# Kernel optimization log

Measured on AMD Instinct MI355X. Metric: run time of the kernel, lower is better.

## Reference

```python
import jax, jax.numpy as jnp
import numpy as np

ALPHA = 0.95   # membrane leak factor exp(-dt/tau_mem)
RHO   = 0.98   # threshold-adaptation decay
BETA  = 1.8    # adaptive threshold gain (ALIF)
TH0   = 1.0    # base threshold
SCALE = 10.0   # SuperSpike surrogate slope

@jax.custom_vjp
def spike(v):
    # Heaviside spike with SuperSpike surrogate gradient (as in cantata's SurrGradSpike)
    return (v >= 0.0).astype(v.dtype)

def _spike_fwd(v):
    return spike(v), v

def _spike_bwd(v, g):
    return (g / (SCALE * jnp.abs(v) + 1.0) ** 2,)

spike.defvjp(_spike_fwd, _spike_bwd)

def _onehot_delays(k, n, d):
    # each presynaptic source is routed through exactly one delay bin
    idx = jax.random.randint(k, (n,), 0, d)
    return (jnp.arange(d)[:, None] == idx[None, :]).astype(jnp.float32)  # [d, n]

def setup_inputs() -> dict:
    B, N, D, NE, DE = 32, 4096, 8, 2048, 4
    key = jax.random.key(0)
    ks = jax.random.split(key, 8)
    V = jax.random.normal(ks[0], (B, N), jnp.float32)
    a = jax.random.uniform(ks[1], (B, N), jnp.float32)
    Xd = (jax.random.uniform(ks[2], (D, B, N)) < 0.05).astype(jnp.float32)      # internal delay ring buffer
    Xext = (jax.random.uniform(ks[3], (DE, B, NE)) < 0.05).astype(jnp.float32)  # delayed external spikes
    W_int = jax.random.normal(ks[4], (N, N), jnp.float32) * 0.02
    W_ext = jax.random.normal(ks[5], (NE, N), jnp.float32) * 0.02
    dmap_int = _onehot_delays(ks[6], N, D)
    dmap_ext = _onehot_delays(ks[7], NE, DE)
    return dict(V=V, a=a, Xd=Xd, Xext=Xext, W_int=W_int, W_ext=W_ext,
                dmap_int=dmap_int, dmap_ext=dmap_ext)

def reference(V, a, Xd, Xext, W_int, W_ext, dmap_int, dmap_ext):
    # 1) ALIF spike generation from membrane + adaptive threshold
    th = TH0 + BETA * a
    X = spike(V - th)                                     # [B,N]
    a_new = RHO * a + X
    # 2) push new spikes into the delay ring buffer (delay 0 = current step)
    Xd_new = jnp.concatenate([X[None], Xd[:-1]], axis=0)  # [D,B,N]
    # 3) delay-mapped synaptic current: gather each presyn source from its delay bin,
    #    then dense delta-synapse accumulation (internal + cross-area)
    x_int = jnp.einsum('dbi,di->bi', Xd_new, dmap_int)    # [B,N]
    x_ext = jnp.einsum('dbi,di->bi', Xext, dmap_ext)      # [B,NE]
    current = x_int @ W_int + x_ext @ W_ext               # [B,N]
    # 4) membrane update: leak, reset on spike, integrate current
    V_new = ALPHA * V * (1.0 - X) + current
    return jnp.stack([X, V_new, a_new])                   # [3,B,N]
```

## Files before the change

kernel.cpp:

```cpp
#include <hip/hip_runtime.h>


#define B_   32
#define N_   4096
#define D_   8
#define NE_  2048
#define DE_  4
#define BN_  (B_ * N_)
#define BNE_ (B_ * NE_)
#define NCH_ 8
#define CI_  512
#define CE_  256

__global__ __launch_bounds__(256) void snn_spike_compact(
    const float* __restrict__ V, const float* __restrict__ a,
    const float* __restrict__ Xd, const float* __restrict__ Xext,
    const float* __restrict__ dmap_int, const float* __restrict__ dmap_ext,
    float* __restrict__ out,
    int* __restrict__ cnt_int, int* __restrict__ cnt_ext,
    unsigned short* __restrict__ list_int, unsigned short* __restrict__ list_ext)
{
#pragma clang fp contract(off)
    __shared__ unsigned short s_i[CI_];
    __shared__ unsigned short s_e[CE_];
    __shared__ int lc_i, lc_e;
    int tid = threadIdx.x;
    if (tid == 0) { lc_i = 0; lc_e = 0; }
    __syncthreads();

    int b = blockIdx.y;
    int c = blockIdx.x;

    #pragma unroll
    for (int r = 0; r < 2; ++r) {
        int i = c * CI_ + r * 256 + tid;
        int t = b * N_ + i;
        float av = a[t];
        float vv = V[t];
        float th = 1.0f + 1.8f * av;
        float x = (vv - th >= 0.0f) ? 1.0f : 0.0f;
        out[t] = x;
        out[2 * BN_ + t] = 0.98f * av + x;
        int di = 0;
        #pragma unroll
        for (int d = 1; d < D_; ++d)
            if (dmap_int[d * N_ + i] != 0.0f) di = d;
        float xi = (di == 0) ? x : Xd[(di - 1) * BN_ + t];
        if (xi != 0.0f) {
            int p = atomicAdd(&lc_i, 1);
            s_i[p] = (unsigned short)i;
        }
    }
    {
        int j = c * CE_ + tid;
        int u = b * NE_ + j;
        int de = 0;
        #pragma unroll
        for (int d = 1; d < DE_; ++d)
            if (dmap_ext[d * NE_ + j] != 0.0f) de = d;
        float xe = Xext[de * BNE_ + u];
        if (xe != 0.0f) {
            int p = atomicAdd(&lc_e, 1);
            s_e[p] = (unsigned short)j;
        }
    }
    __syncthreads();
    if (tid == 0) {
        cnt_int[b * NCH_ + c] = lc_i;
        cnt_ext[b * NCH_ + c] = lc_e;
    }
    for (int k = tid; k < lc_i; k += 256) list_int[b * N_  + c * CI_ + k] = s_i[k];
    for (int k = tid; k < lc_e; k += 256) list_ext[b * NE_ + c * CE_ + k] = s_e[k];
}

__device__ __forceinline__ float4 ld4(const float* p) { return *(const float4*)p; }
__device__ __forceinline__ void add4(float4& a, const float4 w) {
    a.x += w.x; a.y += w.y; a.z += w.z; a.w += w.w;
}

__device__ __forceinline__ void accum_rows(const float* __restrict__ W,
                                           const unsigned short* sl, int n, int j,
                                           float4& acc)
{
    if (n <= 0) return;
    int nf = n & ~7;
    if (nf >= 8) {
        uint4 g = *(const uint4*)(sl);
        float4 p0 = ld4(W + (size_t)(g.x & 0xffff) * N_ + j);
        float4 p1 = ld4(W + (size_t)(g.x >> 16)    * N_ + j);
        float4 p2 = ld4(W + (size_t)(g.y & 0xffff) * N_ + j);
        float4 p3 = ld4(W + (size_t)(g.y >> 16)    * N_ + j);
        float4 p4 = ld4(W + (size_t)(g.z & 0xffff) * N_ + j);
        float4 p5 = ld4(W + (size_t)(g.z >> 16)    * N_ + j);
        float4 p6 = ld4(W + (size_t)(g.w & 0xffff) * N_ + j);
        float4 p7 = ld4(W + (size_t)(g.w >> 16)    * N_ + j);
        for (int k = 8; k < nf; k += 8) {
            uint4 g2 = *(const uint4*)(sl + k);
            float4 q0 = ld4(W + (size_t)(g2.x & 0xffff) * N_ + j);
            float4 q1 = ld4(W + (size_t)(g2.x >> 16)    * N_ + j);
            float4 q2 = ld4(W + (size_t)(g2.y & 0xffff) * N_ + j);
            float4 q3 = ld4(W + (size_t)(g2.y >> 16)    * N_ + j);
            float4 q4 = ld4(W + (size_t)(g2.z & 0xffff) * N_ + j);
            float4 q5 = ld4(W + (size_t)(g2.z >> 16)    * N_ + j);
            float4 q6 = ld4(W + (size_t)(g2.w & 0xffff) * N_ + j);
            float4 q7 = ld4(W + (size_t)(g2.w >> 16)    * N_ + j);
            add4(acc, p0); add4(acc, p1); add4(acc, p2); add4(acc, p3);
            add4(acc, p4); add4(acc, p5); add4(acc, p6); add4(acc, p7);
            p0 = q0; p1 = q1; p2 = q2; p3 = q3;
            p4 = q4; p5 = q5; p6 = q6; p7 = q7;
        }
        add4(acc, p0); add4(acc, p1); add4(acc, p2); add4(acc, p3);
        add4(acc, p4); add4(acc, p5); add4(acc, p6); add4(acc, p7);
    }
    for (int k = nf; k < n; ++k) {
        float4 w = ld4(W + (size_t)sl[k] * N_ + j);
        add4(acc, w);
    }
}

__global__ __launch_bounds__(256) void snn_current(
    const float* __restrict__ W_int, const float* __restrict__ W_ext,
    const float* __restrict__ V, float* __restrict__ out,
    const int* __restrict__ cnt_int, const int* __restrict__ cnt_ext,
    const unsigned short* __restrict__ list_int,
    const unsigned short* __restrict__ list_ext)
{
    __shared__ __align__(16) unsigned short s_int[N_];
    __shared__ __align__(16) unsigned short s_ext[NE_];
    __shared__ float4 s_part[4][64];
    int tid = threadIdx.x;
    int b = blockIdx.y;

    int ci[NCH_], oi[NCH_], ce[NCH_], oe[NCH_];
    int ni = 0, ne = 0;
    #pragma unroll
    for (int c = 0; c < NCH_; ++c) {
        ci[c] = cnt_int[b * NCH_ + c]; oi[c] = ni; ni += ci[c];
        ce[c] = cnt_ext[b * NCH_ + c]; oe[c] = ne; ne += ce[c];
    }
    #pragma unroll
    for (int c = 0; c < NCH_; ++c) {
        for (int k = tid; k < ci[c]; k += 256) s_int[oi[c] + k] = list_int[b * N_  + c * CI_ + k];
        for (int k = tid; k < ce[c]; k += 256) s_ext[oe[c] + k] = list_ext[b * NE_ + c * CE_ + k];
    }
    __syncthreads();

    int w = tid >> 6, lane = tid & 63;
    int j = blockIdx.x * 256 + lane * 4;
    float4 acc = make_float4(0.f, 0.f, 0.f, 0.f);

    int qi = ((ni + 31) >> 5) << 3;
    int si = w * qi;
    accum_rows(W_int, s_int + si, min(ni, si + qi) - si, j, acc);
    int qe = ((ne + 31) >> 5) << 3;
    int se = w * qe;
    accum_rows(W_ext, s_ext + se, min(ne, se + qe) - se, j, acc);

    s_part[w][lane] = acc;
    __syncthreads();
    if (w == 0) {
        float4 a0 = s_part[0][lane], a1 = s_part[1][lane];
        float4 a2 = s_part[2][lane], a3 = s_part[3][lane];
        float4 cur;
        cur.x = (a0.x + a1.x) + (a2.x + a3.x);
        cur.y = (a0.y + a1.y) + (a2.y + a3.y);
        cur.z = (a0.z + a1.z) + (a2.z + a3.z);
        cur.w = (a0.w + a1.w) + (a2.w + a3.w);
        int t = b * N_ + j;
        float4 v = ld4(V + t);
        float4 x = ld4(out + t);
        float4 vn;
        vn.x = 0.95f * v.x * (1.0f - x.x) + cur.x;
        vn.y = 0.95f * v.y * (1.0f - x.y) + cur.y;
        vn.z = 0.95f * v.z * (1.0f - x.z) + cur.z;
        vn.w = 0.95f * v.w * (1.0f - x.w) + cur.w;
        *(float4*)(out + BN_ + t) = vn;
    }
}

extern "C" void kernel_launch(void* const* d_in, const int* in_sizes, int n_in,
                              void* d_out, int out_size, void* d_ws, size_t ws_size,
                              hipStream_t stream)
{
    const float* V        = (const float*)d_in[0];
    const float* a        = (const float*)d_in[1];
    const float* Xd       = (const float*)d_in[2];
    const float* Xext     = (const float*)d_in[3];
    const float* W_int    = (const float*)d_in[4];
    const float* W_ext    = (const float*)d_in[5];
    const float* dmap_int = (const float*)d_in[6];
    const float* dmap_ext = (const float*)d_in[7];
    float* out = (float*)d_out;

    int* cnt_int = (int*)d_ws;
    int* cnt_ext = (int*)((char*)d_ws + 1024);
    unsigned short* list_int = (unsigned short*)((char*)d_ws + 2048);
    unsigned short* list_ext = (unsigned short*)((char*)d_ws + 2048 + (size_t)BN_ * 2);

    dim3 g1(NCH_, B_);
    snn_spike_compact<<<g1, 256, 0, stream>>>(
        V, a, Xd, Xext, dmap_int, dmap_ext, out, cnt_int, cnt_ext, list_int, list_ext);

    dim3 g2(16, B_);
    snn_current<<<g2, 256, 0, stream>>>(
        W_int, W_ext, V, out, cnt_int, cnt_ext, list_int, list_ext);
}
```

Measured before the change: 145.9 us.

## Compact spikes with wavefront ballots over 64-neuron chunks instead of shared atomics

Result: slower. 152.2 us (+4.3%).

```diff
diff --git a/kernel.cpp b/kernel.cpp
--- a/kernel.cpp
+++ b/kernel.cpp
@@ -8,9 +8,13 @@
 #define DE_  4
 #define BN_  (B_ * N_)
 #define BNE_ (B_ * NE_)
-#define NCH_ 8
-#define CI_  512
-#define CE_  256
+#define NCHI 64
+#define NCHE 32
+
+__device__ __forceinline__ float4 ld4(const float* p) { return *(const float4*)p; }
+__device__ __forceinline__ void add4(float4& a, const float4 w) {
+    a.x += w.x; a.y += w.y; a.z += w.z; a.w += w.w;
+}
 
 __global__ __launch_bounds__(256) void snn_spike_compact(
     const float* __restrict__ V, const float* __restrict__ a,
@@ -21,61 +25,61 @@
     unsigned short* __restrict__ list_int, unsigned short* __restrict__ list_ext)
 {
 #pragma clang fp contract(off)
-    __shared__ unsigned short s_i[CI_];
-    __shared__ unsigned short s_e[CE_];
-    __shared__ int lc_i, lc_e;
     int tid = threadIdx.x;
-    if (tid == 0) { lc_i = 0; lc_e = 0; }
-    __syncthreads();
-
-    int b = blockIdx.y;
+    int lane = tid & 63;
+    int o = tid >> 6;
     int c = blockIdx.x;
-
-    #pragma unroll
-    for (int r = 0; r < 2; ++r) {
-        int i = c * CI_ + r * 256 + tid;
-        int t = b * N_ + i;
-        float av = a[t];
-        float vv = V[t];
-        float th = 1.0f + 1.8f * av;
-        float x = (vv - th >= 0.0f) ? 1.0f : 0.0f;
-        out[t] = x;
-        out[2 * BN_ + t] = 0.98f * av + x;
+    if (c < NCHI) {
+        int i = c * 64 + lane;
         int di = 0;
         #pragma unroll
         for (int d = 1; d < D_; ++d)
             if (dmap_int[d * N_ + i] != 0.0f) di = d;
-        float xi = (di == 0) ? x : Xd[(di - 1) * BN_ + t];
-        if (xi != 0.0f) {
-            int p = atomicAdd(&lc_i, 1);
-            s_i[p] = (unsigned short)i;
-        }
-    }
-    {
-        int j = c * CE_ + tid;
-        int u = b * NE_ + j;
+        unsigned m = 0;
+        #pragma unroll
+        for (int bb = 0; bb < 8; ++bb) {
+            int b = o * 8 + bb;
+            int t = b * N_ + i;
+            float av = a[t];
+            float vv = V[t];
+            float th = 1.0f + 1.8f * av;
+            float x = (vv - th >= 0.0f) ? 1.0f : 0.0f;
+            out[t] = x;
+            out[2 * BN_ + t] = 0.98f * av + x;
+            float xi = (di == 0) ? x : Xd[(size_t)(di - 1) * BN_ + t];
+            if (xi != 0.0f) m |= 1u << bb;
+        }
+        #pragma unroll
+        for (int bb = 0; bb < 8; ++bb) {
+            int b = o * 8 + bb;
+            unsigned long long bal = __ballot((m >> bb) & 1u);
+            int pos = __popcll(bal & ((1ull << lane) - 1ull));
+            if ((m >> bb) & 1u) list_int[b * N_ + c * 64 + pos] = (unsigned short)i;
+            if (lane == 0) cnt_int[b * NCHI + c] = (int)__popcll(bal);
+        }
+    } else {
+        int cc = c - NCHI;
+        int j = cc * 64 + lane;
         int de = 0;
         #pragma unroll
         for (int d = 1; d < DE_; ++d)
             if (dmap_ext[d * NE_ + j] != 0.0f) de = d;
-        float xe = Xext[de * BNE_ + u];
-        if (xe != 0.0f) {
-            int p = atomicAdd(&lc_e, 1);
-            s_e[p] = (unsigned short)j;
-        }
-    }
-    __syncthreads();
-    if (tid == 0) {
-        cnt_int[b * NCH_ + c] = lc_i;
-        cnt_ext[b * NCH_ + c] = lc_e;
-    }
-    for (int k = tid; k < lc_i; k += 256) list_int[b * N_  + c * CI_ + k] = s_i[k];
-    for (int k = tid; k < lc_e; k += 256) list_ext[b * NE_ + c * CE_ + k] = s_e[k];
-}
-
-__device__ __forceinline__ float4 ld4(const float* p) { return *(const float4*)p; }
-__device__ __forceinline__ void add4(float4& a, const float4 w) {
-    a.x += w.x; a.y += w.y; a.z += w.z; a.w += w.w;
+        unsigned m = 0;
+        #pragma unroll
+        for (int bb = 0; bb < 8; ++bb) {
+            int b = o * 8 + bb;
+            float xe = Xext[(size_t)de * BNE_ + b * NE_ + j];
+            if (xe != 0.0f) m |= 1u << bb;
+        }
+        #pragma unroll
+        for (int bb = 0; bb < 8; ++bb) {
+            int b = o * 8 + bb;
+            unsigned long long bal = __ballot((m >> bb) & 1u);
+            int pos = __popcll(bal & ((1ull << lane) - 1ull));
+            if ((m >> bb) & 1u) list_ext[b * NE_ + cc * 64 + pos] = (unsigned short)j;
+            if (lane == 0) cnt_ext[b * NCHE + cc] = (int)__popcll(bal);
+        }
+    }
 }
 
 __device__ __forceinline__ void accum_rows(const float* __restrict__ W,
@@ -118,7 +122,7 @@
     }
 }
 
-__global__ __launch_bounds__(256) void snn_current(
+__global__ __launch_bounds__(256, 2) void snn_current(
     const float* __restrict__ W_int, const float* __restrict__ W_ext,
     const float* __restrict__ V, float* __restrict__ out,
     const int* __restrict__ cnt_int, const int* __restrict__ cnt_ext,
@@ -127,26 +131,40 @@
 {
     __shared__ __align__(16) unsigned short s_int[N_];
     __shared__ __align__(16) unsigned short s_ext[NE_];
-    __shared__ float4 s_part[4][64];
+    __shared__ int s_oi[NCHI + 1], s_oe[NCHE + 1];
+    __shared__ float4 s_red[4][64];
+
     int tid = threadIdx.x;
+    int w = tid >> 6, lane = tid & 63;
+    int tile = blockIdx.x;
     int b = blockIdx.y;
 
-    int ci[NCH_], oi[NCH_], ce[NCH_], oe[NCH_];
-    int ni = 0, ne = 0;
+    if (tid == 0) {
+        int s = 0; s_oi[0] = 0;
+        for (int c = 0; c < NCHI; ++c) { s += cnt_int[b * NCHI + c]; s_oi[c + 1] = s; }
+    } else if (tid == 64) {
+        int s = 0; s_oe[0] = 0;
+        for (int c = 0; c < NCHE; ++c) { s += cnt_ext[b * NCHE + c]; s_oe[c + 1] = s; }
+    }
+    __syncthreads();
     #pragma unroll
-    for (int c = 0; c < NCH_; ++c) {
-        ci[c] = cnt_int[b * NCH_ + c]; oi[c] = ni; ni += ci[c];
-        ce[c] = cnt_ext[b * NCH_ + c]; oe[c] = ne; ne += ce[c];
+    for (int r = 0; r < (NCHI * 64) / 256; ++r) {
+        int idx = r * 256 + tid;
+        int c = idx >> 6, ss = idx & 63;
+        int base = s_oi[c];
+        if (ss < s_oi[c + 1] - base) s_int[base + ss] = list_int[b * N_ + idx];
     }
     #pragma unroll
-    for (int c = 0; c < NCH_; ++c) {
-        for (int k = tid; k < ci[c]; k += 256) s_int[oi[c] + k] = list_int[b * N_  + c * CI_ + k];
-        for (int k = tid; k < ce[c]; k += 256) s_ext[oe[c] + k] = list_ext[b * NE_ + c * CE_ + k];
+    for (int r = 0; r < (NCHE * 64) / 256; ++r) {
+        int idx = r * 256 + tid;
+        int c = idx >> 6, ss = idx & 63;
+        int base = s_oe[c];
+        if (ss < s_oe[c + 1] - base) s_ext[base + ss] = list_ext[b * NE_ + idx];
     }
     __syncthreads();
-
-    int w = tid >> 6, lane = tid & 63;
-    int j = blockIdx.x * 256 + lane * 4;
+    int ni = s_oi[NCHI], ne = s_oe[NCHE];
+
+    int j = tile * 256 + lane * 4;
     float4 acc = make_float4(0.f, 0.f, 0.f, 0.f);
 
     int qi = ((ni + 31) >> 5) << 3;
@@ -156,11 +174,11 @@
     int se = w * qe;
     accum_rows(W_ext, s_ext + se, min(ne, se + qe) - se, j, acc);
 
-    s_part[w][lane] = acc;
+    s_red[w][lane] = acc;
     __syncthreads();
     if (w == 0) {
-        float4 a0 = s_part[0][lane], a1 = s_part[1][lane];
-        float4 a2 = s_part[2][lane], a3 = s_part[3][lane];
+        float4 a0 = s_red[0][lane], a1 = s_red[1][lane];
+        float4 a2 = s_red[2][lane], a3 = s_red[3][lane];
         float4 cur;
         cur.x = (a0.x + a1.x) + (a2.x + a3.x);
         cur.y = (a0.y + a1.y) + (a2.y + a3.y);
@@ -192,14 +210,14 @@
     const float* dmap_ext = (const float*)d_in[7];
     float* out = (float*)d_out;
 
-    int* cnt_int = (int*)d_ws;
-    int* cnt_ext = (int*)((char*)d_ws + 1024);
-    unsigned short* list_int = (unsigned short*)((char*)d_ws + 2048);
-    unsigned short* list_ext = (unsigned short*)((char*)d_ws + 2048 + (size_t)BN_ * 2);
-
-    dim3 g1(NCH_, B_);
-    snn_spike_compact<<<g1, 256, 0, stream>>>(
-        V, a, Xd, Xext, dmap_int, dmap_ext, out, cnt_int, cnt_ext, list_int, list_ext);
+    int*            cnt_int  = (int*)d_ws;
+    int*            cnt_ext  = (int*)((char*)d_ws + 8192);
+    unsigned short* list_int = (unsigned short*)((char*)d_ws + 12288);
+    unsigned short* list_ext = (unsigned short*)((char*)d_ws + 274432);
+
+    snn_spike_compact<<<NCHI + NCHE, 256, 0, stream>>>(
+        V, a, Xd, Xext, dmap_int, dmap_ext, out,
+        cnt_int, cnt_ext, list_int, list_ext);
 
     dim3 g2(16, B_);
     snn_current<<<g2, 256, 0, stream>>>(
```
